# Kernel optimization log

Hardware: AMD Instinct MI355X
Metric: run time of the kernel (lower is better)

The kernel has to match this reference:

```python
import jax, jax.numpy as jnp
import numpy as np

N = 50000      # nodes
E = 800000     # edges (avg degree 16)
IN = 256       # in_dim == heads*hidden (so DGL residual is Identity)
H = 4          # heads
D = 64         # hidden_dim / out_dim per head
EPS = 1e-5
NEG_SLOPE_ATTN = 0.2   # DGL GATConv edge-attention leaky_relu slope
NEG_SLOPE_ACT = 0.01   # F.leaky_relu default


def gat_conv(x, src, dst, W, al, ar, b, act):
    # x: [N, H*D], W: [H*D, H*D], al/ar: [H, D], b: [H*D]
    feat = (x @ W).reshape(N, H, D)                       # [N,H,D]
    el = jnp.sum(feat * al, axis=-1)                      # [N,H]
    er = jnp.sum(feat * ar, axis=-1)                      # [N,H]
    e = jax.nn.leaky_relu(el[src] + er[dst], NEG_SLOPE_ATTN)  # [E,H]
    # segment softmax over incoming edges per destination node
    m = jax.ops.segment_max(e, dst, num_segments=N)       # [N,H]
    m = jnp.where(jnp.isfinite(m), m, 0.0)                # nodes with no in-edges
    ee = jnp.exp(e - m[dst])                              # [E,H]
    denom = jax.ops.segment_sum(ee, dst, num_segments=N)  # [N,H]
    alpha = ee / jnp.maximum(denom[dst], 1e-9)            # [E,H]
    msg = feat[src] * alpha[:, :, None]                   # [E,H,D]
    rst = jax.ops.segment_sum(msg, dst, num_segments=N)   # [N,H,D]
    rst = rst + x.reshape(N, H, D)                        # identity residual (dims match)
    rst = rst + b.reshape(1, H, D)
    if act:
        rst = jax.nn.leaky_relu(rst, NEG_SLOPE_ACT)
    return rst


def batch_norm(h, gamma, beta):
    # BatchNorm1d in training mode: batch statistics over node dim
    mu = jnp.mean(h, axis=0)
    var = jnp.var(h, axis=0)
    return (h - mu) * jax.lax.rsqrt(var + EPS) * gamma + beta


def setup_inputs():
    key = jax.random.key(0)
    ks = jax.random.split(key, 18)
    s = 1.0 / np.sqrt(IN)
    inp = {
        'x': jax.random.normal(ks[0], (N, IN), jnp.float32),
        'src': jax.random.randint(ks[1], (E,), 0, N),
        'dst': jax.random.randint(ks[2], (E,), 0, N),
    }
    names = ['W1', 'al1', 'ar1', 'b1', 'W2', 'al2', 'ar2', 'b2', 'W3', 'al3', 'ar3', 'b3']
    shapes = [(IN, H * D), (H, D), (H, D), (H * D,)] * 3
    for i, (nm, sh) in enumerate(zip(names, shapes)):
        inp[nm] = jax.random.normal(ks[3 + i], sh, jnp.float32) * s
    inp['g1'] = jnp.ones((H * D,), jnp.float32)
    inp['be1'] = jnp.zeros((H * D,), jnp.float32)
    inp['g2'] = jnp.ones((H * D,), jnp.float32)
    inp['be2'] = jnp.zeros((H * D,), jnp.float32)
    return inp


def reference(x, src, dst, W1, al1, ar1, b1, W2, al2, ar2, b2, W3, al3, ar3, b3, g1, be1, g2, be2):
    h = gat_conv(x, src, dst, W1, al1, ar1, b1, act=True).reshape(N, H * D)
    h = batch_norm(h, g1, be1)
    h = gat_conv(h, src, dst, W2, al2, ar2, b2, act=True).reshape(N, H * D)
    h = batch_norm(h, g2, be2)
    h = gat_conv(h, src, dst, W3, al3, ar3, b3, act=False)   # [N,H,D]
    return h.mean(axis=1)                                    # [N,D]
```

## Files before the change

### kernel.cpp

```cpp
#include <hip/hip_runtime.h>

constexpr int NN = 50000;
constexpr int NE = 800000;
constexpr float SLOPE_A = 0.2f;
constexpr float SLOPE_R = 0.01f;
constexpr int SCB = 196;

typedef __attribute__((ext_vector_type(8))) short bf16x8;
typedef __attribute__((ext_vector_type(4))) float f32x4;

__device__ __forceinline__ unsigned short f2bf(float f) {
    union { float f; unsigned u; } v; v.f = f;
    unsigned u = v.u;
    unsigned r = u + 0x7fffu + ((u >> 16) & 1u);
    return (unsigned short)(r >> 16);
}
__device__ __forceinline__ float bf2f(unsigned short s) {
    union { unsigned u; float f; } v; v.u = ((unsigned)s) << 16;
    return v.f;
}

__global__ void k_hist(const int* __restrict__ dst, int* __restrict__ cnt) {
    int i = blockIdx.x * 256 + threadIdx.x;
    if (i < NE) atomicAdd(&cnt[dst[i]], 1);
}

__global__ void k_scan1(const int* __restrict__ cnt, int* __restrict__ loc,
                        int* __restrict__ bsum) {
    __shared__ int sh[256];
    int t = threadIdx.x;
    int i = blockIdx.x * 256 + t;
    int v = (i < NN) ? cnt[i] : 0;
    sh[t] = v;
    __syncthreads();
    for (int off = 1; off < 256; off <<= 1) {
        int tmp = (t >= off) ? sh[t - off] : 0;
        __syncthreads();
        sh[t] += tmp;
        __syncthreads();
    }
    loc[i] = sh[t] - v;
    if (t == 255) bsum[blockIdx.x] = sh[255];
}

__global__ void k_scan2(const int* __restrict__ bsum, int* __restrict__ boff,
                        int* __restrict__ rowptr) {
    __shared__ int sh[256];
    int t = threadIdx.x;
    int v = (t < SCB) ? bsum[t] : 0;
    sh[t] = v;
    __syncthreads();
    for (int off = 1; off < 256; off <<= 1) {
        int tmp = (t >= off) ? sh[t - off] : 0;
        __syncthreads();
        sh[t] += tmp;
        __syncthreads();
    }
    if (t < SCB) boff[t] = sh[t] - v;
    if (t == 255) rowptr[NN] = sh[255];
}

__global__ void k_scan3(const int* __restrict__ loc, const int* __restrict__ boff,
                        int* __restrict__ rowptr, int* __restrict__ cursor) {
    int i = blockIdx.x * 256 + threadIdx.x;
    if (i < NN) {
        int r = loc[i] + boff[blockIdx.x];
        rowptr[i] = r;
        cursor[i] = r;
    }
}

__global__ void k_scatter(const int* __restrict__ src, const int* __restrict__ dst,
                          int* __restrict__ cursor, int* __restrict__ ssrc) {
    int i = blockIdx.x * 256 + threadIdx.x;
    if (i < NE) {
        int d = dst[i];
        int pos = atomicAdd(&cursor[d], 1);
        ssrc[pos] = src[i];
    }
}

__global__ void k_prepw(const float* __restrict__ W1, const float* __restrict__ W2,
                        const float* __restrict__ W3, unsigned short* __restrict__ Wt) {
    int b = blockIdx.x;
    int L = b >> 8, k = b & 255;
    const float* W = (L == 0) ? W1 : ((L == 1) ? W2 : W3);
    int j = threadIdx.x;
    Wt[L * 65536 + j * 256 + k] = f2bf(W[k * 256 + j]);
}

__launch_bounds__(256, 2)
__global__ void k_gemm(const float* __restrict__ A, const unsigned short* __restrict__ Wt,
                       const float* __restrict__ bnscale, const float* __restrict__ bnshift,
                       int use_bn, const float* __restrict__ al, const float* __restrict__ ar,
                       unsigned short* __restrict__ feat16, float* __restrict__ el,
                       float* __restrict__ er) {
    constexpr int AP = 264;
    __shared__ __align__(16) unsigned short Alds[64 * AP];
    const int tid = threadIdx.x;
    const int rowbase = blockIdx.x * 64;

    {
        int r = tid >> 6;
        int c4 = tid & 63;
        for (int it = 0; it < 16; it++) {
            int rr = it * 4 + r;
            int gr = rowbase + rr;
            float4 v = make_float4(0.f, 0.f, 0.f, 0.f);
            if (gr < NN) v = *(const float4*)(A + (size_t)gr * 256 + c4 * 4);
            if (use_bn) {
                float4 sc = *(const float4*)(bnscale + c4 * 4);
                float4 sh = *(const float4*)(bnshift + c4 * 4);
                v.x = v.x * sc.x + sh.x;
                v.y = v.y * sc.y + sh.y;
                v.z = v.z * sc.z + sh.z;
                v.w = v.w * sc.w + sh.w;
            }
            ushort4 pv;
            pv.x = f2bf(v.x); pv.y = f2bf(v.y); pv.z = f2bf(v.z); pv.w = f2bf(v.w);
            *(ushort4*)(&Alds[rr * AP + c4 * 4]) = pv;
        }
    }
    __syncthreads();

    f32x4 acc[4][4];
    for (int i = 0; i < 4; i++)
        for (int j = 0; j < 4; j++)
            acc[i][j] = (f32x4){0.f, 0.f, 0.f, 0.f};

    const int lane = tid & 63, w = tid >> 6;
    const int mm = lane & 15, q = lane >> 4;

    const unsigned short* bbase = Wt + ((size_t)(64 * w + mm)) * 256 + q * 8;

#pragma unroll
    for (int kc = 0; kc < 8; kc++) {
        bf16x8 a[4], b[4];
        for (int i = 0; i < 4; i++)
            a[i] = *(const bf16x8*)(&Alds[(16 * i + mm) * AP + kc * 32 + q * 8]);
        for (int j = 0; j < 4; j++)
            b[j] = *(const bf16x8*)(bbase + j * (16 * 256) + kc * 32);
        for (int i = 0; i < 4; i++)
            for (int j = 0; j < 4; j++)
                acc[i][j] = __builtin_amdgcn_mfma_f32_16x16x32_bf16(a[i], b[j], acc[i][j], 0, 0, 0);
    }

    float alv[4], arv[4];
    for (int j = 0; j < 4; j++) {
        alv[j] = al[w * 64 + 16 * j + mm];
        arv[j] = ar[w * 64 + 16 * j + mm];
    }
    for (int i = 0; i < 4; i++) {
        for (int r = 0; r < 4; r++) {
            int gr = rowbase + 16 * i + q * 4 + r;
            float se = 0.f, sr = 0.f;
            for (int j = 0; j < 4; j++) {
                se += acc[i][j][r] * alv[j];
                sr += acc[i][j][r] * arv[j];
            }
            for (int off = 1; off < 16; off <<= 1) {
                se += __shfl_xor(se, off, 64);
                sr += __shfl_xor(sr, off, 64);
            }
            if (mm == 0 && gr < NN) {
                el[gr * 4 + w] = se;
                er[gr * 4 + w] = sr;
            }
        }
    }

    for (int i = 0; i < 4; i++) {
        for (int j = 0; j < 4; j++) {
            int gc = 64 * w + 16 * j + mm;
            for (int r = 0; r < 4; r++) {
                int gr = rowbase + 16 * i + q * 4 + r;
                if (gr < NN) feat16[(size_t)gr * 256 + gc] = f2bf(acc[i][j][r]);
            }
        }
    }
}

__launch_bounds__(256)
__global__ void k_agg(const unsigned short* __restrict__ feat16, const float* __restrict__ el,
                      const float* __restrict__ er, const int* __restrict__ rowptr,
                      const int* __restrict__ ssrc, const float* __restrict__ resid,
                      const float* __restrict__ bnscale, const float* __restrict__ bnshift,
                      int use_bn, const float* __restrict__ bias, int act,
                      float* __restrict__ out, int final_mean) {
    int n = __builtin_amdgcn_readfirstlane(blockIdx.x * 4 + (threadIdx.x >> 6));
    int l = threadIdx.x & 63;
    int h = l >> 4;
    int beg = rowptr[n], end = rowptr[n + 1];
    float erh = er[n * 4 + h];

    float d = 0.f;
    float4 acc = make_float4(0.f, 0.f, 0.f, 0.f);

    for (int e = beg; e < end; e += 8) {
        int ss[8];
        float cc[8];
        ushort4 ff[8];
#pragma unroll
        for (int j = 0; j < 8; j++) {
            int ee = e + j;
            ss[j] = ssrc[(ee < end) ? ee : beg];
        }
#pragma unroll
        for (int j = 0; j < 8; j++)
            cc[j] = el[ss[j] * 4 + h];
#pragma unroll
        for (int j = 0; j < 8; j++)
            ff[j] = *(const ushort4*)(feat16 + (size_t)ss[j] * 256 + l * 4);
#pragma unroll
        for (int j = 0; j < 8; j++) {
            float sc = cc[j] + erh;
            sc = (sc > 0.f) ? sc : SLOPE_A * sc;
            float wgt = ((e + j) < end) ? __expf(sc) : 0.f;
            d += wgt;
            acc.x += bf2f(ff[j].x) * wgt;
            acc.y += bf2f(ff[j].y) * wgt;
            acc.z += bf2f(ff[j].z) * wgt;
            acc.w += bf2f(ff[j].w) * wgt;
        }
    }

    float invd = 1.f / fmaxf(d, 1e-9f);
    acc.x *= invd; acc.y *= invd; acc.z *= invd; acc.w *= invd;

    float4 r = *(const float4*)(resid + (size_t)n * 256 + l * 4);
    if (use_bn) {
        float4 sc4 = *(const float4*)(bnscale + l * 4);
        float4 sh4 = *(const float4*)(bnshift + l * 4);
        r.x = r.x * sc4.x + sh4.x;
        r.y = r.y * sc4.y + sh4.y;
        r.z = r.z * sc4.z + sh4.z;
        r.w = r.w * sc4.w + sh4.w;
    }
    float4 bb = *(const float4*)(bias + l * 4);
    acc.x += r.x + bb.x; acc.y += r.y + bb.y;
    acc.z += r.z + bb.z; acc.w += r.w + bb.w;
    if (act) {
        acc.x = (acc.x > 0.f) ? acc.x : SLOPE_R * acc.x;
        acc.y = (acc.y > 0.f) ? acc.y : SLOPE_R * acc.y;
        acc.z = (acc.z > 0.f) ? acc.z : SLOPE_R * acc.z;
        acc.w = (acc.w > 0.f) ? acc.w : SLOPE_R * acc.w;
    }

    if (!final_mean) {
        *(float4*)(out + (size_t)n * 256 + l * 4) = acc;
    } else {
        acc.x += __shfl_xor(acc.x, 16, 64); acc.x += __shfl_xor(acc.x, 32, 64);
        acc.y += __shfl_xor(acc.y, 16, 64); acc.y += __shfl_xor(acc.y, 32, 64);
        acc.z += __shfl_xor(acc.z, 16, 64); acc.z += __shfl_xor(acc.z, 32, 64);
        acc.w += __shfl_xor(acc.w, 16, 64); acc.w += __shfl_xor(acc.w, 32, 64);
        if (l < 16) {
            acc.x *= 0.25f; acc.y *= 0.25f; acc.z *= 0.25f; acc.w *= 0.25f;
            *(float4*)(out + (size_t)n * 64 + l * 4) = acc;
        }
    }
}

__global__ void k_bnstats(const float* __restrict__ hh, float* __restrict__ sums) {
    int t = threadIdx.x;
    int b = blockIdx.x;
    int r0 = b * 196, r1 = min(r0 + 196, NN);
    float s = 0.f, s2 = 0.f;
    for (int r = r0; r < r1; r++) {
        float v = hh[(size_t)r * 256 + t];
        s += v; s2 += v * v;
    }
    atomicAdd(&sums[t], s);
    atomicAdd(&sums[256 + t], s2);
}

__global__ void k_bnfinal(const float* __restrict__ sums, const float* __restrict__ g,
                          const float* __restrict__ be, float* __restrict__ scale,
                          float* __restrict__ shift) {
    int t = threadIdx.x;
    float mu = sums[t] * (1.f / NN);
    float var = sums[256 + t] * (1.f / NN) - mu * mu;
    float rs = rsqrtf(var + 1e-5f);
    float sc = rs * g[t];
    scale[t] = sc;
    shift[t] = be[t] - mu * sc;
}

extern "C" void kernel_launch(void* const* d_in, const int* in_sizes, int n_in,
                              void* d_out, int out_size, void* d_ws, size_t ws_size,
                              hipStream_t stream) {
    const float* x   = (const float*)d_in[0];
    const int* src   = (const int*)d_in[1];
    const int* dst   = (const int*)d_in[2];
    const float* W1  = (const float*)d_in[3];
    const float* al1 = (const float*)d_in[4];
    const float* ar1 = (const float*)d_in[5];
    const float* b1  = (const float*)d_in[6];
    const float* W2  = (const float*)d_in[7];
    const float* al2 = (const float*)d_in[8];
    const float* ar2 = (const float*)d_in[9];
    const float* b2  = (const float*)d_in[10];
    const float* W3  = (const float*)d_in[11];
    const float* al3 = (const float*)d_in[12];
    const float* ar3 = (const float*)d_in[13];
    const float* b3  = (const float*)d_in[14];
    const float* g1  = (const float*)d_in[15];
    const float* be1 = (const float*)d_in[16];
    const float* g2  = (const float*)d_in[17];
    const float* be2 = (const float*)d_in[18];
    float* out = (float*)d_out;

    char* ws = (char*)d_ws;
    size_t off = 0;
    auto alloc = [&](size_t bytes) {
        void* p = ws + off;
        off += (bytes + 255) & ~(size_t)255;
        return p;
    };
    int* rowptr = (int*)alloc((NN + 1) * sizeof(int));
    int* cursor = (int*)alloc(NN * sizeof(int));
    int* cnt    = (int*)alloc(SCB * 256 * sizeof(int));
    int* loc    = (int*)alloc(SCB * 256 * sizeof(int));
    int* bsum   = (int*)alloc(SCB * sizeof(int));
    int* boff   = (int*)alloc(SCB * sizeof(int));
    int* ssrc   = (int*)alloc(NE * sizeof(int));
    unsigned short* feat16 = (unsigned short*)alloc((size_t)NN * 256 * sizeof(unsigned short));
    float* hbuf = (float*)alloc((size_t)NN * 256 * sizeof(float));
    float* el   = (float*)alloc((size_t)NN * 4 * sizeof(float));
    float* er   = (float*)alloc((size_t)NN * 4 * sizeof(float));
    unsigned short* Wt = (unsigned short*)alloc(3 * 65536 * sizeof(unsigned short));
    float* bnsums  = (float*)alloc(512 * sizeof(float));
    float* bnscale = (float*)alloc(256 * sizeof(float));
    float* bnshift = (float*)alloc(256 * sizeof(float));

    hipMemsetAsync(cnt, 0, NN * sizeof(int), stream);
    k_hist<<<(NE + 255) / 256, 256, 0, stream>>>(dst, cnt);
    k_scan1<<<SCB, 256, 0, stream>>>(cnt, loc, bsum);
    k_scan2<<<1, 256, 0, stream>>>(bsum, boff, rowptr);
    k_scan3<<<SCB, 256, 0, stream>>>(loc, boff, rowptr, cursor);
    k_scatter<<<(NE + 255) / 256, 256, 0, stream>>>(src, dst, cursor, ssrc);
    k_prepw<<<768, 256, 0, stream>>>(W1, W2, W3, Wt);

    const int GB = (NN + 63) / 64;
    const int NB = NN / 4;

    k_gemm<<<GB, 256, 0, stream>>>(x, Wt, nullptr, nullptr, 0, al1, ar1, feat16, el, er);
    k_agg<<<NB, 256, 0, stream>>>(feat16, el, er, rowptr, ssrc, x,
                                  nullptr, nullptr, 0, b1, 1, hbuf, 0);
    hipMemsetAsync(bnsums, 0, 512 * sizeof(float), stream);
    k_bnstats<<<256, 256, 0, stream>>>(hbuf, bnsums);
    k_bnfinal<<<1, 256, 0, stream>>>(bnsums, g1, be1, bnscale, bnshift);

    k_gemm<<<GB, 256, 0, stream>>>(hbuf, Wt + 65536, bnscale, bnshift, 1, al2, ar2, feat16, el, er);
    k_agg<<<NB, 256, 0, stream>>>(feat16, el, er, rowptr, ssrc, hbuf,
                                  bnscale, bnshift, 1, b2, 1, hbuf, 0);
    hipMemsetAsync(bnsums, 0, 512 * sizeof(float), stream);
    k_bnstats<<<256, 256, 0, stream>>>(hbuf, bnsums);
    k_bnfinal<<<1, 256, 0, stream>>>(bnsums, g2, be2, bnscale, bnshift);

    k_gemm<<<GB, 256, 0, stream>>>(hbuf, Wt + 131072, bnscale, bnshift, 1, al3, ar3, feat16, el, er);
    k_agg<<<NB, 256, 0, stream>>>(feat16, el, er, rowptr, ssrc, hbuf,
                                  bnscale, bnshift, 1, b3, 0, out, 1);
}
```

Measured before the change: 615.8 us.

## Store intermediate activations in bf16 and fold BatchNorm into GEMM weights

Hidden activations (hbuf) and the input x are now kept in bf16 rather than fp32, which halves the bytes read and written by the GEMM A-load, the residual read in aggregation and the BN-stats pass. The BatchNorm scale is folded into a per-layer copy of the weight matrix and the shift into a per-column bias vector (cvec) by a new k_fold kernel, so the GEMM A-load becomes a plain bf16 copy. This adds an x-cast kernel and three small fold kernels. Residuals and BN statistics now carry bf16 rounding, which may cost accuracy.

Result: slower. 629.8 us (+2.3%).

```diff
diff --git a/kernel.cpp b/kernel.cpp
--- a/kernel.cpp
+++ b/kernel.cpp
@@ -89,10 +89,36 @@
     Wt[L * 65536 + j * 256 + k] = f2bf(W[k * 256 + j]);
 }
 
+__global__ void k_xcast(const float* __restrict__ x, unsigned short* __restrict__ xbf) {
+    size_t i = (size_t)blockIdx.x * 256 + threadIdx.x;
+    float4 v = *(const float4*)(x + i * 4);
+    ushort4 p;
+    p.x = f2bf(v.x); p.y = f2bf(v.y); p.z = f2bf(v.z); p.w = f2bf(v.w);
+    *(ushort4*)(xbf + i * 4) = p;
+}
+
+__global__ void k_fold(const unsigned short* __restrict__ Wsrc, const float* __restrict__ sc,
+                       const float* __restrict__ sh, unsigned short* __restrict__ Wt2,
+                       float* __restrict__ cvec) {
+    __shared__ float red[256];
+    int j = blockIdx.x, k = threadIdx.x;
+    float w = bf2f(Wsrc[j * 256 + k]);
+    float s = sc ? sc[k] : 1.f;
+    float hs = sh ? sh[k] : 0.f;
+    Wt2[j * 256 + k] = f2bf(s * w);
+    red[k] = hs * w;
+    __syncthreads();
+    for (int off = 128; off > 0; off >>= 1) {
+        if (k < off) red[k] += red[k + off];
+        __syncthreads();
+    }
+    if (k == 0) cvec[j] = red[0];
+}
+
 __launch_bounds__(256, 2)
-__global__ void k_gemm(const float* __restrict__ A, const unsigned short* __restrict__ Wt,
-                       const float* __restrict__ bnscale, const float* __restrict__ bnshift,
-                       int use_bn, const float* __restrict__ al, const float* __restrict__ ar,
+__global__ void k_gemm(const unsigned short* __restrict__ A, const unsigned short* __restrict__ Wt,
+                       const float* __restrict__ cvec,
+                       const float* __restrict__ al, const float* __restrict__ ar,
                        unsigned short* __restrict__ feat16, float* __restrict__ el,
                        float* __restrict__ er) {
     constexpr int AP = 264;
@@ -100,26 +126,14 @@
     const int tid = threadIdx.x;
     const int rowbase = blockIdx.x * 64;
 
-    {
-        int r = tid >> 6;
-        int c4 = tid & 63;
-        for (int it = 0; it < 16; it++) {
-            int rr = it * 4 + r;
-            int gr = rowbase + rr;
-            float4 v = make_float4(0.f, 0.f, 0.f, 0.f);
-            if (gr < NN) v = *(const float4*)(A + (size_t)gr * 256 + c4 * 4);
-            if (use_bn) {
-                float4 sc = *(const float4*)(bnscale + c4 * 4);
-                float4 sh = *(const float4*)(bnshift + c4 * 4);
-                v.x = v.x * sc.x + sh.x;
-                v.y = v.y * sc.y + sh.y;
-                v.z = v.z * sc.z + sh.z;
-                v.w = v.w * sc.w + sh.w;
-            }
-            ushort4 pv;
-            pv.x = f2bf(v.x); pv.y = f2bf(v.y); pv.z = f2bf(v.z); pv.w = f2bf(v.w);
-            *(ushort4*)(&Alds[rr * AP + c4 * 4]) = pv;
-        }
+    for (int it = 0; it < 8; it++) {
+        int idx = it * 256 + tid;
+        int rr = idx >> 5;
+        int c16 = idx & 31;
+        int gr = rowbase + rr;
+        uint4 v = make_uint4(0u, 0u, 0u, 0u);
+        if (gr < NN) v = *(const uint4*)(A + (size_t)gr * 256 + c16 * 8);
+        *(uint4*)(&Alds[rr * AP + c16 * 8]) = v;
     }
     __syncthreads();
 
@@ -144,6 +158,13 @@
             for (int j = 0; j < 4; j++)
                 acc[i][j] = __builtin_amdgcn_mfma_f32_16x16x32_bf16(a[i], b[j], acc[i][j], 0, 0, 0);
     }
+
+    float cv[4];
+    for (int j = 0; j < 4; j++) cv[j] = cvec[64 * w + 16 * j + mm];
+    for (int i = 0; i < 4; i++)
+        for (int j = 0; j < 4; j++)
+            for (int r = 0; r < 4; r++)
+                acc[i][j][r] += cv[j];
 
     float alv[4], arv[4];
     for (int j = 0; j < 4; j++) {
@@ -183,10 +204,11 @@
 __launch_bounds__(256)
 __global__ void k_agg(const unsigned short* __restrict__ feat16, const float* __restrict__ el,
                       const float* __restrict__ er, const int* __restrict__ rowptr,
-                      const int* __restrict__ ssrc, const float* __restrict__ resid,
+                      const int* __restrict__ ssrc, const unsigned short* __restrict__ resid,
                       const float* __restrict__ bnscale, const float* __restrict__ bnshift,
                       int use_bn, const float* __restrict__ bias, int act,
-                      float* __restrict__ out, int final_mean) {
+                      unsigned short* __restrict__ outh, float* __restrict__ outf,
+                      int final_mean) {
     int n = __builtin_amdgcn_readfirstlane(blockIdx.x * 4 + (threadIdx.x >> 6));
     int l = threadIdx.x & 63;
     int h = l >> 4;
@@ -227,7 +249,8 @@
     float invd = 1.f / fmaxf(d, 1e-9f);
     acc.x *= invd; acc.y *= invd; acc.z *= invd; acc.w *= invd;
 
-    float4 r = *(const float4*)(resid + (size_t)n * 256 + l * 4);
+    ushort4 rv = *(const ushort4*)(resid + (size_t)n * 256 + l * 4);
+    float4 r = make_float4(bf2f(rv.x), bf2f(rv.y), bf2f(rv.z), bf2f(rv.w));
     if (use_bn) {
         float4 sc4 = *(const float4*)(bnscale + l * 4);
         float4 sh4 = *(const float4*)(bnshift + l * 4);
@@ -247,7 +270,9 @@
     }
 
     if (!final_mean) {
-        *(float4*)(out + (size_t)n * 256 + l * 4) = acc;
+        ushort4 p;
+        p.x = f2bf(acc.x); p.y = f2bf(acc.y); p.z = f2bf(acc.z); p.w = f2bf(acc.w);
+        *(ushort4*)(outh + (size_t)n * 256 + l * 4) = p;
     } else {
         acc.x += __shfl_xor(acc.x, 16, 64); acc.x += __shfl_xor(acc.x, 32, 64);
         acc.y += __shfl_xor(acc.y, 16, 64); acc.y += __shfl_xor(acc.y, 32, 64);
@@ -255,18 +280,18 @@
         acc.w += __shfl_xor(acc.w, 16, 64); acc.w += __shfl_xor(acc.w, 32, 64);
         if (l < 16) {
             acc.x *= 0.25f; acc.y *= 0.25f; acc.z *= 0.25f; acc.w *= 0.25f;
-            *(float4*)(out + (size_t)n * 64 + l * 4) = acc;
-        }
-    }
-}
-
-__global__ void k_bnstats(const float* __restrict__ hh, float* __restrict__ sums) {
+            *(float4*)(outf + (size_t)n * 64 + l * 4) = acc;
+        }
+    }
+}
+
+__global__ void k_bnstats(const unsigned short* __restrict__ hh, float* __restrict__ sums) {
     int t = threadIdx.x;
     int b = blockIdx.x;
     int r0 = b * 196, r1 = min(r0 + 196, NN);
     float s = 0.f, s2 = 0.f;
     for (int r = r0; r < r1; r++) {
-        float v = hh[(size_t)r * 256 + t];
+        float v = bf2f(hh[(size_t)r * 256 + t]);
         s += v; s2 += v * v;
     }
     atomicAdd(&sums[t], s);
@@ -323,16 +348,20 @@
     int* bsum   = (int*)alloc(SCB * sizeof(int));
     int* boff   = (int*)alloc(SCB * sizeof(int));
     int* ssrc   = (int*)alloc(NE * sizeof(int));
+    unsigned short* xbf    = (unsigned short*)alloc((size_t)NN * 256 * sizeof(unsigned short));
     unsigned short* feat16 = (unsigned short*)alloc((size_t)NN * 256 * sizeof(unsigned short));
-    float* hbuf = (float*)alloc((size_t)NN * 256 * sizeof(float));
+    unsigned short* hbuf   = (unsigned short*)alloc((size_t)NN * 256 * sizeof(unsigned short));
     float* el   = (float*)alloc((size_t)NN * 4 * sizeof(float));
     float* er   = (float*)alloc((size_t)NN * 4 * sizeof(float));
-    unsigned short* Wt = (unsigned short*)alloc(3 * 65536 * sizeof(unsigned short));
+    unsigned short* Wt  = (unsigned short*)alloc(3 * 65536 * sizeof(unsigned short));
+    unsigned short* Wt2 = (unsigned short*)alloc(65536 * sizeof(unsigned short));
+    float* cvec    = (float*)alloc(256 * sizeof(float));
     float* bnsums  = (float*)alloc(512 * sizeof(float));
     float* bnscale = (float*)alloc(256 * sizeof(float));
     float* bnshift = (float*)alloc(256 * sizeof(float));
 
     hipMemsetAsync(cnt, 0, NN * sizeof(int), stream);
+    k_xcast<<<12500, 256, 0, stream>>>(x, xbf);
     k_hist<<<(NE + 255) / 256, 256, 0, stream>>>(dst, cnt);
     k_scan1<<<SCB, 256, 0, stream>>>(cnt, loc, bsum);
     k_scan2<<<1, 256, 0, stream>>>(bsum, boff, rowptr);
@@ -343,21 +372,24 @@
     const int GB = (NN + 63) / 64;
     const int NB = NN / 4;
 
-    k_gemm<<<GB, 256, 0, stream>>>(x, Wt, nullptr, nullptr, 0, al1, ar1, feat16, el, er);
-    k_agg<<<NB, 256, 0, stream>>>(feat16, el, er, rowptr, ssrc, x,
-                                  nullptr, nullptr, 0, b1, 1, hbuf, 0);
+    k_fold<<<256, 256, 0, stream>>>(Wt, nullptr, nullptr, Wt2, cvec);
+    k_gemm<<<GB, 256, 0, stream>>>(xbf, Wt2, cvec, al1, ar1, feat16, el, er);
+    k_agg<<<NB, 256, 0, stream>>>(feat16, el, er, rowptr, ssrc, xbf,
+                                  nullptr, nullptr, 0, b1, 1, hbuf, nullptr, 0);
     hipMemsetAsync(bnsums, 0, 512 * sizeof(float), stream);
     k_bnstats<<<256, 256, 0, stream>>>(hbuf, bnsums);
     k_bnfinal<<<1, 256, 0, stream>>>(bnsums, g1, be1, bnscale, bnshift);
 
-    k_gemm<<<GB, 256, 0, stream>>>(hbuf, Wt + 65536, bnscale, bnshift, 1, al2, ar2, feat16, el, er);
+    k_fold<<<256, 256, 0, stream>>>(Wt + 65536, bnscale, bnshift, Wt2, cvec);
+    k_gemm<<<GB, 256, 0, stream>>>(hbuf, Wt2, cvec, al2, ar2, feat16, el, er);
     k_agg<<<NB, 256, 0, stream>>>(feat16, el, er, rowptr, ssrc, hbuf,
-                                  bnscale, bnshift, 1, b2, 1, hbuf, 0);
+                                  bnscale, bnshift, 1, b2, 1, hbuf, nullptr, 0);
     hipMemsetAsync(bnsums, 0, 512 * sizeof(float), stream);
     k_bnstats<<<256, 256, 0, stream>>>(hbuf, bnsums);
     k_bnfinal<<<1, 256, 0, stream>>>(bnsums, g2, be2, bnscale, bnshift);
 
-    k_gemm<<<GB, 256, 0, stream>>>(hbuf, Wt + 131072, bnscale, bnshift, 1, al3, ar3, feat16, el, er);
+    k_fold<<<256, 256, 0, stream>>>(Wt + 131072, bnscale, bnshift, Wt2, cvec);
+    k_gemm<<<GB, 256, 0, stream>>>(hbuf, Wt2, cvec, al3, ar3, feat16, el, er);
     k_agg<<<NB, 256, 0, stream>>>(feat16, el, er, rowptr, ssrc, hbuf,
-                                  bnscale, bnshift, 1, b3, 0, out, 1);
-}
+                                  bnscale, bnshift, 1, b3, 0, nullptr, out, 1);
+}
```
